# Optimization experiments

Hardware: AMD Instinct MI355X
Metric: run time of the kernel (lower is better)

Reference implementation:

```python
import jax, jax.numpy as jnp
import numpy as np

EMBED = 1024
HEADS = 16
HEAD_DIM = EMBED // HEADS
B, S = 4, 2048


def setup_inputs() -> dict:
    key = jax.random.key(0)
    ks = jax.random.split(key, 13)
    std = 1.0 / np.sqrt(EMBED)
    inp = {
        "q": jax.random.normal(ks[0], (B, S, EMBED), jnp.float32),
        "k": jax.random.normal(ks[1], (B, S, EMBED), jnp.float32),
        "v": jax.random.normal(ks[2], (B, S, EMBED), jnp.float32),
        "mask": jax.random.randint(ks[3], (B, 1, S, S), 0, 2, jnp.int32),
        "wq_w": jax.random.normal(ks[4], (EMBED, EMBED), jnp.float32) * std,
        "wq_b": jax.random.normal(ks[5], (EMBED,), jnp.float32) * std,
        "wk_w": jax.random.normal(ks[6], (EMBED, EMBED), jnp.float32) * std,
        "wk_b": jax.random.normal(ks[7], (EMBED,), jnp.float32) * std,
        "wv_w": jax.random.normal(ks[8], (EMBED, EMBED), jnp.float32) * std,
        "wv_b": jax.random.normal(ks[9], (EMBED,), jnp.float32) * std,
        "fo_w": jax.random.normal(ks[10], (EMBED, EMBED), jnp.float32) * std,
        "fo_b": jax.random.normal(ks[11], (EMBED,), jnp.float32) * std,
    }
    return inp


def reference(q, k, v, mask, wq_w, wq_b, wk_w, wk_b, wv_w, wv_b, fo_w, fo_b):
    N = q.shape[0]
    # linear projections (torch Linear: x @ W.T + b)
    qp = (q @ wq_w.T + wq_b).reshape(N, -1, HEADS, HEAD_DIM)
    kp = (k @ wk_w.T + wk_b).reshape(N, -1, HEADS, HEAD_DIM)
    vp = (v @ wv_w.T + wv_b).reshape(N, -1, HEADS, HEAD_DIM)
    # [N, H, Q, K] scores
    energy = jnp.einsum('nqhd,nkhd->nhqk', qp, kp)
    energy = jnp.where(mask == 0, jnp.float32(-1e20), energy)
    # NOTE: original scales by sqrt(embed_size), not sqrt(head_dim)
    attention = jax.nn.softmax(energy / np.float32(np.sqrt(EMBED)), axis=3)
    out = jnp.einsum('nhql,nlhd->nqhd', attention, vp).reshape(N, -1, EMBED)
    return out @ fo_w.T + fo_b
```

## Files before the change

### kernel.cpp

```cpp
#include <hip/hip_runtime.h>

typedef __attribute__((ext_vector_type(4))) float f32x4;
typedef __attribute__((ext_vector_type(16))) float f32x16;
typedef __attribute__((ext_vector_type(8))) __bf16 bf16x8;
typedef __attribute__((ext_vector_type(8))) unsigned short ushort8;
typedef __attribute__((ext_vector_type(4))) unsigned short ushort4v;
typedef __attribute__((ext_vector_type(4))) unsigned uint4v;

#define EMBED 1024
#define SEQ   2048
#define BATCH 4
#define HEADS 16
#define HDIM  64
#define SCL 0.045084220027780106f

#define GLD_LDS16(g, l) __builtin_amdgcn_global_load_lds( \
    (const __attribute__((address_space(1))) void*)(g),   \
    (__attribute__((address_space(3))) void*)(l), 16, 0, 0)

static __device__ __forceinline__ unsigned short f2bf(float f) {
  unsigned u = __builtin_bit_cast(unsigned, f);
  u += 0x7FFFu + ((u >> 16) & 1u);
  return (unsigned short)(u >> 16);
}
static __device__ __forceinline__ unsigned cvtpk(float a, float b) {
  unsigned r;
  asm("v_cvt_pk_bf16_f32 %0, %1, %2" : "=v"(r) : "v"(a), "v"(b));
  return r;
}

__global__ __launch_bounds__(256) void pack_mask_kernel(
    const int* __restrict__ m, unsigned long long* __restrict__ out) {
  int t = blockIdx.x * 256 + threadIdx.x;
  unsigned long long bits = __ballot(m[t] != 0);
  if ((threadIdx.x & 63) == 0) out[t >> 6] = bits;
}

__global__ __launch_bounds__(256) void cvt_kernel(
    const float* __restrict__ s, unsigned short* __restrict__ d, int nvec) {
  int i = blockIdx.x * 256 + threadIdx.x;
  if (i >= nvec) return;
  f32x4 a = ((const f32x4*)s)[2 * i];
  f32x4 b = ((const f32x4*)s)[2 * i + 1];
  ushort8 o;
#pragma unroll
  for (int j = 0; j < 4; ++j) { o[j] = f2bf(a[j]); o[4 + j] = f2bf(b[j]); }
  ((ushort8*)d)[i] = o;
}

template<int OUT_MODE>
__global__ __launch_bounds__(256) void gemm_bt(
    const unsigned short* __restrict__ A, const unsigned short* __restrict__ B,
    const float* __restrict__ bias, void* __restrict__ outp) {
  __shared__ unsigned short Ab[2][128 * 32];
  __shared__ unsigned short Bb[2][128 * 32];
  const int tid = threadIdx.x, lane = tid & 63, wv = tid >> 6;
  const int wy = wv >> 1, wx = wv & 1, ln = lane & 15, g = lane >> 4;
  const int mbase = blockIdx.x * 128, nbase = blockIdx.y * 128;

  const int srow = tid >> 2, scol = (tid & 3) * 16;
  const char* Ag = (const char*)(A + (size_t)(mbase + srow) * EMBED) + scol;
  const char* Bg = (const char*)(B + (size_t)(nbase + srow) * EMBED) + scol;
  const size_t R64 = (size_t)64 * EMBED * 2;

  f32x4 acc[4][4];
#pragma unroll
  for (int i = 0; i < 4; i++)
#pragma unroll
    for (int j = 0; j < 4; j++) acc[i][j] = (f32x4){0.f, 0.f, 0.f, 0.f};

  auto STAGE = [&](int buf, int kt) {
    const size_t koff = (size_t)kt * 64;
    char* al = (char*)&Ab[buf][0] + tid * 16;
    char* bl = (char*)&Bb[buf][0] + tid * 16;
    GLD_LDS16(Ag + koff, al);
    GLD_LDS16(Ag + koff + R64, al + 4096);
    GLD_LDS16(Bg + koff, bl);
    GLD_LDS16(Bg + koff + R64, bl + 4096);
  };

  STAGE(0, 0);
  const int NT = EMBED / 32;
  for (int kt = 0; kt < NT; ++kt) {
    __syncthreads();
    const int cur = kt & 1;
    if (kt + 1 < NT) STAGE(cur ^ 1, kt + 1);
    bf16x8 af[4], bfr[4];
#pragma unroll
    for (int ms = 0; ms < 4; ++ms)
      af[ms] = __builtin_bit_cast(bf16x8,
          *(const ushort8*)&Ab[cur][(wy * 64 + ms * 16 + ln) * 32 + g * 8]);
#pragma unroll
    for (int ns = 0; ns < 4; ++ns)
      bfr[ns] = __builtin_bit_cast(bf16x8,
          *(const ushort8*)&Bb[cur][(wx * 64 + ns * 16 + ln) * 32 + g * 8]);
#pragma unroll
    for (int ms = 0; ms < 4; ++ms)
#pragma unroll
      for (int ns = 0; ns < 4; ++ns)
        acc[ms][ns] = __builtin_amdgcn_mfma_f32_16x16x32_bf16(
            af[ms], bfr[ns], acc[ms][ns], 0, 0, 0);
  }

  float bv[4];
#pragma unroll
  for (int ns = 0; ns < 4; ++ns) bv[ns] = bias[nbase + wx * 64 + ns * 16 + ln];

  if (OUT_MODE == 0) {
    unsigned short* out = (unsigned short*)outp;
#pragma unroll
    for (int ms = 0; ms < 4; ++ms)
#pragma unroll
      for (int ns = 0; ns < 4; ++ns) {
        int col = nbase + wx * 64 + ns * 16 + ln;
#pragma unroll
        for (int j = 0; j < 4; ++j) {
          int row = mbase + wy * 64 + ms * 16 + g * 4 + j;
          out[(size_t)row * EMBED + col] = f2bf(acc[ms][ns][j] + bv[ns]);
        }
      }
  } else if (OUT_MODE == 1) {
    unsigned short* out = (unsigned short*)outp;
#pragma unroll
    for (int ms = 0; ms < 4; ++ms)
#pragma unroll
      for (int ns = 0; ns < 4; ++ns) {
        int row0 = mbase + wy * 64 + ms * 16 + g * 4;
        int col = nbase + wx * 64 + ns * 16 + ln;
        int b = row0 >> 11, s0 = row0 & (SEQ - 1);
        int h = col >> 6, d = col & 63;
        ushort4v pk;
#pragma unroll
        for (int j = 0; j < 4; ++j) pk[j] = f2bf(acc[ms][ns][j] + bv[ns]);
        *(ushort4v*)&out[(size_t)((b * HEADS + h) * HDIM + d) * SEQ + s0] = pk;
      }
  } else {
    float* out = (float*)outp;
#pragma unroll
    for (int ms = 0; ms < 4; ++ms)
#pragma unroll
      for (int ns = 0; ns < 4; ++ns) {
        int col = nbase + wx * 64 + ns * 16 + ln;
#pragma unroll
        for (int j = 0; j < 4; ++j) {
          int row = mbase + wy * 64 + ms * 16 + g * 4 + j;
          out[(size_t)row * EMBED + col] = acc[ms][ns][j] + bv[ns];
        }
      }
  }
}

__global__ __launch_bounds__(512, 4) void attn4_kernel(
    const unsigned short* __restrict__ qp, const unsigned short* __restrict__ kp,
    const unsigned short* __restrict__ vpT,
    const unsigned long long* __restrict__ mask64,
    unsigned short* __restrict__ attb) {
  __shared__ unsigned char lds[32768];
  unsigned char* Kb = lds;
  unsigned char* Vb = lds + 16384;

  const int tid = threadIdx.x;
  const int lane = tid & 63;
  const int lo = lane & 31, hi = lane >> 5;

  const int flat = blockIdx.x + 8 * blockIdx.y + 128 * blockIdx.z;
  const int bh = (flat & 7) * 8 + ((flat >> 3) & 7);
  const int qc = flat >> 6;
  const int b = bh >> 4, h = bh & 15;
  const int qb = qc * 256 + (tid >> 6) * 32;
  const int q = qb + lo;

  bf16x8 qf[4];
  {
    const unsigned short* qr = qp + (size_t)(b * SEQ + q) * EMBED + h * HDIM + hi * 8;
#pragma unroll
    for (int c = 0; c < 4; ++c) {
      ushort8 u = *(const ushort8*)(qr + 16 * c);
      bf16x8 f;
#pragma unroll
      for (int j = 0; j < 8; ++j) {
        float x = __builtin_bit_cast(float, (unsigned)u[j] << 16) * SCL;
        f[j] = (__bf16)x;
      }
      qf[c] = f;
    }
  }

  const int srow = tid >> 3;
  const int srcc = ((tid & 7) * 16) ^ (((tid >> 3) & 7) << 4);
  const char* kbase = (const char*)kp
      + ((size_t)(b * SEQ + srow) * EMBED + h * HDIM) * 2 + srcc;
  const char* vbase = (const char*)vpT
      + ((size_t)((b * HEADS + h) * HDIM + srow)) * SEQ * 2 + srcc;

  auto STAGE = [&](int buf, int kt) {
    GLD_LDS16(kbase + (size_t)kt * 64 * EMBED * 2, Kb + buf * 8192 + tid * 16);
    GLD_LDS16(vbase + (size_t)kt * 128, Vb + buf * 8192 + tid * 16);
  };

  f32x16 oacc0, oacc1, oacc2;
#pragma unroll
  for (int i = 0; i < 16; ++i) { oacc0[i] = 0.f; oacc1[i] = 0.f; oacc2[i] = 0.f; }
  bf16x8 ones;
#pragma unroll
  for (int j = 0; j < 8; ++j) ones[j] = (__bf16)1.0f;

  const unsigned long long* mrow = mask64 + (size_t)(b * SEQ + q) * (SEQ / 64);
  const int swz = (lo & 7) << 4;

  STAGE(0, 0);
  const int NT = SEQ / 64;
  for (int kt = 0; kt < NT; ++kt) {
    const int cur = kt & 1;
    __syncthreads();
    if (kt + 1 < NT) STAGE(cur ^ 1, kt + 1);
    const unsigned long long mw = mrow[kt];
    const unsigned char* Kc = Kb + cur * 8192;
    const unsigned char* Vc = Vb + cur * 8192;

    bf16x8 PA[4];
#pragma unroll
    for (int kg = 0; kg < 2; ++kg) {
      f32x16 e;
#pragma unroll
      for (int i = 0; i < 16; ++i) e[i] = 0.f;
      const int krow = kg * 32 + lo;
#pragma unroll
      for (int c = 0; c < 4; ++c) {
        const int colb = (16 * c + 8 * hi) * 2;
        bf16x8 kf = *(const bf16x8*)(Kc + krow * 128 + (colb ^ swz));
        e = __builtin_amdgcn_mfma_f32_32x32x16_bf16(kf, qf[c], e, 0, 0, 0);
      }
      const unsigned mh = (unsigned)(mw >> (kg * 32 + 4 * hi));
      float p[16];
#pragma unroll
      for (int m = 0; m < 4; ++m)
#pragma unroll
        for (int j = 0; j < 4; ++j) {
          float pe = __builtin_amdgcn_exp2f(e[4 * m + j]);
          p[4 * m + j] = (mh & (1u << (8 * m + j))) ? pe : 0.f;
        }
      unsigned wA0 = cvtpk(p[0], p[1]),   wB0 = cvtpk(p[2], p[3]);
      unsigned wA1 = cvtpk(p[4], p[5]),   wB1 = cvtpk(p[6], p[7]);
      unsigned wA2 = cvtpk(p[8], p[9]),   wB2 = cvtpk(p[10], p[11]);
      unsigned wA3 = cvtpk(p[12], p[13]), wB3 = cvtpk(p[14], p[15]);
      asm("v_permlane32_swap_b32 %0, %1" : "+v"(wA0), "+v"(wA1));
      asm("v_permlane32_swap_b32 %0, %1" : "+v"(wB0), "+v"(wB1));
      asm("v_permlane32_swap_b32 %0, %1" : "+v"(wA2), "+v"(wA3));
      asm("v_permlane32_swap_b32 %0, %1" : "+v"(wB2), "+v"(wB3));
      PA[2 * kg]     = __builtin_bit_cast(bf16x8, (uint4v){wA0, wB0, wA1, wB1});
      PA[2 * kg + 1] = __builtin_bit_cast(bf16x8, (uint4v){wA2, wB2, wA3, wB3});
    }

    __builtin_amdgcn_s_setprio(1);
#pragma unroll
    for (int c = 0; c < 4; ++c) {
      const int pcolb = 32 * c + 16 * hi;
      bf16x8 pf = PA[c];
      {
        bf16x8 vf = *(const bf16x8*)(Vc + lo * 128 + (pcolb ^ swz));
        oacc0 = __builtin_amdgcn_mfma_f32_32x32x16_bf16(pf, vf, oacc0, 0, 0, 0);
      }
      {
        const int drow = 32 + lo;
        bf16x8 vf = *(const bf16x8*)(Vc + drow * 128 + (pcolb ^ swz));
        oacc1 = __builtin_amdgcn_mfma_f32_32x32x16_bf16(pf, vf, oacc1, 0, 0, 0);
      }
      oacc2 = __builtin_amdgcn_mfma_f32_32x32x16_bf16(pf, ones, oacc2, 0, 0, 0);
    }
    __builtin_amdgcn_s_setprio(0);
  }

#pragma unroll
  for (int r = 0; r < 16; ++r) {
    const int qq = qb + (r & 3) + 8 * (r >> 2) + 4 * hi;
    const float dinv = 1.0f / oacc2[r];
    unsigned short* orow = attb + (size_t)(b * SEQ + qq) * EMBED + h * HDIM;
    orow[lo] = f2bf(oacc0[r] * dinv);
    orow[32 + lo] = f2bf(oacc1[r] * dinv);
  }
}

extern "C" void kernel_launch(void* const* d_in, const int* in_sizes, int n_in,
                              void* d_out, int out_size, void* d_ws, size_t ws_size,
                              hipStream_t stream) {
  const float* q    = (const float*)d_in[0];
  const float* k    = (const float*)d_in[1];
  const float* v    = (const float*)d_in[2];
  const int*   mask = (const int*)d_in[3];
  const float* wq_w = (const float*)d_in[4];
  const float* wq_b = (const float*)d_in[5];
  const float* wk_w = (const float*)d_in[6];
  const float* wk_b = (const float*)d_in[7];
  const float* wv_w = (const float*)d_in[8];
  const float* wv_b = (const float*)d_in[9];
  const float* fo_w = (const float*)d_in[10];
  const float* fo_b = (const float*)d_in[11];

  char* ws = (char*)d_ws;
  const size_t MB = 1024 * 1024;
  unsigned short* stage = (unsigned short*)(ws);
  unsigned short* wqb   = (unsigned short*)(ws + 16 * MB);
  unsigned short* wkb   = (unsigned short*)(ws + 18 * MB);
  unsigned short* wvb   = (unsigned short*)(ws + 20 * MB);
  unsigned short* fob   = (unsigned short*)(ws + 22 * MB);
  unsigned short* qp    = (unsigned short*)(ws + 24 * MB);
  unsigned short* kp    = (unsigned short*)(ws + 40 * MB);
  unsigned short* vpT   = (unsigned short*)(ws + 56 * MB);
  unsigned long long* m64 = (unsigned long long*)(ws + 72 * MB);

  const int NVX = BATCH * SEQ * EMBED / 8;
  const int NVW = EMBED * EMBED / 8;

  pack_mask_kernel<<<(BATCH * SEQ * SEQ) / 256, 256, 0, stream>>>(mask, m64);

  cvt_kernel<<<NVW / 256, 256, 0, stream>>>(wq_w, wqb, NVW);
  cvt_kernel<<<NVW / 256, 256, 0, stream>>>(wk_w, wkb, NVW);
  cvt_kernel<<<NVW / 256, 256, 0, stream>>>(wv_w, wvb, NVW);
  cvt_kernel<<<NVW / 256, 256, 0, stream>>>(fo_w, fob, NVW);

  dim3 gg((BATCH * SEQ) / 128, EMBED / 128);
  cvt_kernel<<<NVX / 256, 256, 0, stream>>>(q, stage, NVX);
  gemm_bt<0><<<gg, 256, 0, stream>>>(stage, wqb, wq_b, qp);
  cvt_kernel<<<NVX / 256, 256, 0, stream>>>(k, stage, NVX);
  gemm_bt<0><<<gg, 256, 0, stream>>>(stage, wkb, wk_b, kp);
  cvt_kernel<<<NVX / 256, 256, 0, stream>>>(v, stage, NVX);
  gemm_bt<1><<<gg, 256, 0, stream>>>(stage, wvb, wv_b, vpT);

  attn4_kernel<<<dim3(8, HEADS, BATCH), 512, 0, stream>>>(qp, kp, vpT, m64, stage);

  gemm_bt<2><<<gg, 256, 0, stream>>>(stage, fob, fo_b, (float*)d_out);
}
```

Measured before the change: 285.6 us.

## Triple-buffer GEMM and attention loads, stage mask via LDS, batch weight conversions

Both the projection GEMM and the attention kernel move from double to triple buffering. Each uses a single raw barrier plus explicit vmcnt waits, so two tiles are in flight while one is computed. The attention kernel now stages the packed mask words into LDS through async global-to-LDS loads instead of a per-thread global load on each iteration. The four weight conversions are merged into one launch. This uses more LDS per block, which may lower occupancy, and correctness depends on the hand-tuned vmcnt counts.

```diff
diff --git a/kernel.cpp b/kernel.cpp
--- a/kernel.cpp
+++ b/kernel.cpp
@@ -17,6 +17,9 @@
 #define GLD_LDS16(g, l) __builtin_amdgcn_global_load_lds( \
     (const __attribute__((address_space(1))) void*)(g),   \
     (__attribute__((address_space(3))) void*)(l), 16, 0, 0)
+#define GLD_LDS4(g, l) __builtin_amdgcn_global_load_lds(  \
+    (const __attribute__((address_space(1))) void*)(g),   \
+    (__attribute__((address_space(3))) void*)(l), 4, 0, 0)
 
 static __device__ __forceinline__ unsigned short f2bf(float f) {
   unsigned u = __builtin_bit_cast(unsigned, f);
@@ -48,12 +51,29 @@
   ((ushort8*)d)[i] = o;
 }
 
+__global__ __launch_bounds__(256) void cvt4_kernel(
+    const float* __restrict__ s0, const float* __restrict__ s1,
+    const float* __restrict__ s2, const float* __restrict__ s3,
+    unsigned short* __restrict__ d, int nvec) {
+  int i = blockIdx.x * 256 + threadIdx.x;
+  if (i >= nvec) return;
+  const float* s = (blockIdx.y == 0) ? s0 : (blockIdx.y == 1) ? s1
+                 : (blockIdx.y == 2) ? s2 : s3;
+  unsigned short* dd = d + (size_t)blockIdx.y * nvec * 8;
+  f32x4 a = ((const f32x4*)s)[2 * i];
+  f32x4 b = ((const f32x4*)s)[2 * i + 1];
+  ushort8 o;
+#pragma unroll
+  for (int j = 0; j < 4; ++j) { o[j] = f2bf(a[j]); o[4 + j] = f2bf(b[j]); }
+  ((ushort8*)dd)[i] = o;
+}
+
 template<int OUT_MODE>
-__global__ __launch_bounds__(256) void gemm_bt(
+__global__ __launch_bounds__(256, 3) void gemm_bt(
     const unsigned short* __restrict__ A, const unsigned short* __restrict__ B,
     const float* __restrict__ bias, void* __restrict__ outp) {
-  __shared__ unsigned short Ab[2][128 * 32];
-  __shared__ unsigned short Bb[2][128 * 32];
+  __shared__ unsigned short Ab[3 * 128 * 32];
+  __shared__ unsigned short Bb[3 * 128 * 32];
   const int tid = threadIdx.x, lane = tid & 63, wv = tid >> 6;
   const int wy = wv >> 1, wx = wv & 1, ln = lane & 15, g = lane >> 4;
   const int mbase = blockIdx.x * 128, nbase = blockIdx.y * 128;
@@ -71,8 +91,8 @@
 
   auto STAGE = [&](int buf, int kt) {
     const size_t koff = (size_t)kt * 64;
-    char* al = (char*)&Ab[buf][0] + tid * 16;
-    char* bl = (char*)&Bb[buf][0] + tid * 16;
+    char* al = (char*)Ab + buf * 8192 + tid * 16;
+    char* bl = (char*)Bb + buf * 8192 + tid * 16;
     GLD_LDS16(Ag + koff, al);
     GLD_LDS16(Ag + koff + R64, al + 4096);
     GLD_LDS16(Bg + koff, bl);
@@ -80,26 +100,37 @@
   };
 
   STAGE(0, 0);
+  STAGE(1, 1);
   const int NT = EMBED / 32;
+  int buf = 0;
   for (int kt = 0; kt < NT; ++kt) {
-    __syncthreads();
-    const int cur = kt & 1;
-    if (kt + 1 < NT) STAGE(cur ^ 1, kt + 1);
+    __builtin_amdgcn_s_barrier();
+    if (kt + 2 < NT) {
+      int nb = buf + 2; if (nb >= 3) nb -= 3;
+      STAGE(nb, kt + 2);
+      asm volatile("s_waitcnt vmcnt(8)" ::: "memory");
+    } else if (kt + 1 < NT) {
+      asm volatile("s_waitcnt vmcnt(4)" ::: "memory");
+    } else {
+      asm volatile("s_waitcnt vmcnt(0)" ::: "memory");
+    }
+    __builtin_amdgcn_sched_barrier(0);
     bf16x8 af[4], bfr[4];
 #pragma unroll
     for (int ms = 0; ms < 4; ++ms)
       af[ms] = __builtin_bit_cast(bf16x8,
-          *(const ushort8*)&Ab[cur][(wy * 64 + ms * 16 + ln) * 32 + g * 8]);
+          *(const ushort8*)&Ab[buf * 4096 + (wy * 64 + ms * 16 + ln) * 32 + g * 8]);
 #pragma unroll
     for (int ns = 0; ns < 4; ++ns)
       bfr[ns] = __builtin_bit_cast(bf16x8,
-          *(const ushort8*)&Bb[cur][(wx * 64 + ns * 16 + ln) * 32 + g * 8]);
+          *(const ushort8*)&Bb[buf * 4096 + (wx * 64 + ns * 16 + ln) * 32 + g * 8]);
 #pragma unroll
     for (int ms = 0; ms < 4; ++ms)
 #pragma unroll
       for (int ns = 0; ns < 4; ++ns)
         acc[ms][ns] = __builtin_amdgcn_mfma_f32_16x16x32_bf16(
             af[ms], bfr[ns], acc[ms][ns], 0, 0, 0);
+    buf = (buf == 2) ? 0 : buf + 1;
   }
 
   float bv[4];
@@ -150,24 +181,25 @@
   }
 }
 
-__global__ __launch_bounds__(512, 4) void attn4_kernel(
+__global__ __launch_bounds__(512, 4) void attn5_kernel(
     const unsigned short* __restrict__ qp, const unsigned short* __restrict__ kp,
     const unsigned short* __restrict__ vpT,
     const unsigned long long* __restrict__ mask64,
     unsigned short* __restrict__ attb) {
-  __shared__ unsigned char lds[32768];
+  __shared__ unsigned char lds[55296];
   unsigned char* Kb = lds;
-  unsigned char* Vb = lds + 16384;
+  unsigned char* Vb = lds + 24576;
+  unsigned char* Mb = lds + 49152;
 
   const int tid = threadIdx.x;
-  const int lane = tid & 63;
+  const int lane = tid & 63, wv = tid >> 6;
   const int lo = lane & 31, hi = lane >> 5;
 
   const int flat = blockIdx.x + 8 * blockIdx.y + 128 * blockIdx.z;
   const int bh = (flat & 7) * 8 + ((flat >> 3) & 7);
   const int qc = flat >> 6;
   const int b = bh >> 4, h = bh & 15;
-  const int qb = qc * 256 + (tid >> 6) * 32;
+  const int qb = qc * 256 + wv * 32;
   const int q = qb + lo;
 
   bf16x8 qf[4];
@@ -192,10 +224,13 @@
       + ((size_t)(b * SEQ + srow) * EMBED + h * HDIM) * 2 + srcc;
   const char* vbase = (const char*)vpT
       + ((size_t)((b * HEADS + h) * HDIM + srow)) * SEQ * 2 + srcc;
+  const char* mgbase = (const char*)mask64
+      + ((size_t)(b * SEQ + qc * 256 + (tid >> 1)) * 32) * 8 + (tid & 1) * 4;
 
   auto STAGE = [&](int buf, int kt) {
     GLD_LDS16(kbase + (size_t)kt * 64 * EMBED * 2, Kb + buf * 8192 + tid * 16);
     GLD_LDS16(vbase + (size_t)kt * 128, Vb + buf * 8192 + tid * 16);
+    GLD_LDS4(mgbase + kt * 8, Mb + buf * 2048 + tid * 4);
   };
 
   f32x16 oacc0, oacc1, oacc2;
@@ -205,18 +240,28 @@
 #pragma unroll
   for (int j = 0; j < 8; ++j) ones[j] = (__bf16)1.0f;
 
-  const unsigned long long* mrow = mask64 + (size_t)(b * SEQ + q) * (SEQ / 64);
   const int swz = (lo & 7) << 4;
 
   STAGE(0, 0);
+  STAGE(1, 1);
   const int NT = SEQ / 64;
+  int buf = 0;
   for (int kt = 0; kt < NT; ++kt) {
-    const int cur = kt & 1;
-    __syncthreads();
-    if (kt + 1 < NT) STAGE(cur ^ 1, kt + 1);
-    const unsigned long long mw = mrow[kt];
-    const unsigned char* Kc = Kb + cur * 8192;
-    const unsigned char* Vc = Vb + cur * 8192;
+    __builtin_amdgcn_s_barrier();
+    if (kt + 2 < NT) {
+      int nb = buf + 2; if (nb >= 3) nb -= 3;
+      STAGE(nb, kt + 2);
+      asm volatile("s_waitcnt vmcnt(6)" ::: "memory");
+    } else if (kt + 1 < NT) {
+      asm volatile("s_waitcnt vmcnt(3)" ::: "memory");
+    } else {
+      asm volatile("s_waitcnt vmcnt(0)" ::: "memory");
+    }
+    __builtin_amdgcn_sched_barrier(0);
+    const unsigned char* Kc = Kb + buf * 8192;
+    const unsigned char* Vc = Vb + buf * 8192;
+    const unsigned long long mw =
+        *(const unsigned long long*)(Mb + buf * 2048 + (wv * 32 + lo) * 8);
 
     bf16x8 PA[4];
 #pragma unroll
@@ -269,6 +314,7 @@
       oacc2 = __builtin_amdgcn_mfma_f32_32x32x16_bf16(pf, ones, oacc2, 0, 0, 0);
     }
     __builtin_amdgcn_s_setprio(0);
+    buf = (buf == 2) ? 0 : buf + 1;
   }
 
 #pragma unroll
@@ -301,9 +347,6 @@
   const size_t MB = 1024 * 1024;
   unsigned short* stage = (unsigned short*)(ws);
   unsigned short* wqb   = (unsigned short*)(ws + 16 * MB);
-  unsigned short* wkb   = (unsigned short*)(ws + 18 * MB);
-  unsigned short* wvb   = (unsigned short*)(ws + 20 * MB);
-  unsigned short* fob   = (unsigned short*)(ws + 22 * MB);
   unsigned short* qp    = (unsigned short*)(ws + 24 * MB);
   unsigned short* kp    = (unsigned short*)(ws + 40 * MB);
   unsigned short* vpT   = (unsigned short*)(ws + 56 * MB);
@@ -314,10 +357,10 @@
 
   pack_mask_kernel<<<(BATCH * SEQ * SEQ) / 256, 256, 0, stream>>>(mask, m64);
 
-  cvt_kernel<<<NVW / 256, 256, 0, stream>>>(wq_w, wqb, NVW);
-  cvt_kernel<<<NVW / 256, 256, 0, stream>>>(wk_w, wkb, NVW);
-  cvt_kernel<<<NVW / 256, 256, 0, stream>>>(wv_w, wvb, NVW);
-  cvt_kernel<<<NVW / 256, 256, 0, stream>>>(fo_w, fob, NVW);
+  cvt4_kernel<<<dim3(NVW / 256, 4), 256, 0, stream>>>(wq_w, wk_w, wv_w, fo_w, wqb, NVW);
+  unsigned short* wkb = wqb + (size_t)NVW * 8;
+  unsigned short* wvb = wkb + (size_t)NVW * 8;
+  unsigned short* fob = wvb + (size_t)NVW * 8;
 
   dim3 gg((BATCH * SEQ) / 128, EMBED / 128);
   cvt_kernel<<<NVX / 256, 256, 0, stream>>>(q, stage, NVX);
@@ -327,7 +370,7 @@
   cvt_kernel<<<NVX / 256, 256, 0, stream>>>(v, stage, NVX);
   gemm_bt<1><<<gg, 256, 0, stream>>>(stage, wvb, wv_b, vpT);
 
-  attn4_kernel<<<dim3(8, HEADS, BATCH), 512, 0, stream>>>(qp, kp, vpT, m64, stage);
+  attn5_kernel<<<dim3(8, HEADS, BATCH), 512, 0, stream>>>(qp, kp, vpT, m64, stage);
 
   gemm_bt<2><<<gg, 256, 0, stream>>>(stage, fob, fo_b, (float*)d_out);
 }
```

New measurement: 260.8 us. 1.1x faster.
